# Optimization experiments

Measured on AMD Instinct MI355X. Metric: run time of the kernel, lower is better.

Reference implementation:

```python
import jax, jax.numpy as jnp
import numpy as np

N, E, IN_DIM, OUT_DIM, H = 50000, 800000, 128, 16, 8


def setup_inputs() -> dict:
    key = jax.random.key(0)
    ks = jax.random.split(key, 10)
    h = jax.random.normal(ks[0], (N, IN_DIM), dtype=jnp.float32)
    row = jnp.sort(jax.random.randint(ks[1], (E,), 0, N))
    col = jax.random.randint(ks[2], (E,), 0, N)
    s = 1.0 / np.sqrt(IN_DIM)
    Wq = jax.random.normal(ks[3], (IN_DIM, OUT_DIM * H), dtype=jnp.float32) * s
    Wk = jax.random.normal(ks[4], (IN_DIM, OUT_DIM * H), dtype=jnp.float32) * s
    Wv = jax.random.normal(ks[5], (IN_DIM, OUT_DIM * H), dtype=jnp.float32) * s
    bq = jnp.zeros((OUT_DIM * H,), jnp.float32)
    bk = jnp.zeros((OUT_DIM * H,), jnp.float32)
    bv = jnp.zeros((OUT_DIM * H,), jnp.float32)
    return {"h": h, "Wq": Wq, "bq": bq, "Wk": Wk, "bk": bk, "Wv": Wv, "bv": bv,
            "row": row, "col": col}


def reference(h, Wq, bq, Wk, bk, Wv, bv, row, col):
    n = h.shape[0]
    scaling = OUT_DIM ** (-0.5)
    # projections, reshaped (N, out_dim, heads) as in the torch module
    q = (h @ Wq + bq).reshape(n, OUT_DIM, H) * scaling
    k = (h @ Wk + bk).reshape(n, OUT_DIM, H)
    v = (h @ Wv + bv).reshape(n, OUT_DIM, H)
    # bsddmm: per-edge, per-head dot product  score[e,h] = <q[row[e],:,h], k[col[e],:,h]>
    s = jnp.einsum('edh,edh->eh', q[row], k[col])  # [E, H]
    # sparse row-wise softmax (over each destination node's neighbors)
    m = jax.ops.segment_max(s, row, num_segments=n)       # [N, H]
    p = jnp.exp(s - m[row])                               # [E, H]
    z = jax.ops.segment_sum(p, row, num_segments=n)       # [N, H]
    attn = p / z[row]                                     # [E, H]
    # bspmm: out[i,d,h] = sum_{e: row[e]=i} attn[e,h] * v[col[e],d,h]
    out = jax.ops.segment_sum(attn[:, None, :] * v[col], row, num_segments=n)
    return out.reshape(n, -1)
```

## Files before the change

### kernel.cpp

```cpp
#include <hip/hip_runtime.h>
#include <math.h>

typedef unsigned int uint32;
typedef _Float16 f16x8 __attribute__((ext_vector_type(8)));
typedef _Float16 f16x2 __attribute__((ext_vector_type(2)));
typedef float f32x4 __attribute__((ext_vector_type(4)));

union frag_u { f16x8 h; uint32 u[4]; uint4 q; };


__device__ __forceinline__ uint32 pack_f16(float lo, float hi) {
    auto r = __builtin_amdgcn_cvt_pkrtz(lo, hi);
    return __builtin_bit_cast(uint32, r);
}
__device__ __forceinline__ float dot2acc(uint32 a, uint32 b, float c) {
#if __has_builtin(__builtin_amdgcn_fdot2)
    return __builtin_amdgcn_fdot2(__builtin_bit_cast(f16x2, a),
                                  __builtin_bit_cast(f16x2, b), c, false);
#else
    f16x2 av = __builtin_bit_cast(f16x2, a), bv = __builtin_bit_cast(f16x2, b);
    return fmaf((float)av[0], (float)bv[0], fmaf((float)av[1], (float)bv[1], c));
#endif
}

__global__ __launch_bounds__(256) void proj_mfma_kernel(
    const float* __restrict__ h,
    const float* __restrict__ Wq, const float* __restrict__ Wk,
    const float* __restrict__ Wv,
    const float* __restrict__ bq, const float* __restrict__ bk,
    const float* __restrict__ bv,
    uint32* __restrict__ Qp, uint2* __restrict__ KV,
    const int* __restrict__ row, int* __restrict__ rp,
    int N, int E, int PB)
{
    const int t = threadIdx.x;
    if ((int)blockIdx.x >= PB) {
        int i = ((int)blockIdx.x - PB) * 256 + t;
        if (i > N) return;
        int lo = 0, hi = E;
        while (lo < hi) {
            int mid = (lo + hi) >> 1;
            if (row[mid] < i) lo = mid + 1; else hi = mid;
        }
        rp[i] = lo;
        return;
    }

    __shared__ uint32 Wl[8192];

    const int lane = t & 63;
    const int w = t >> 6;
    const int r = lane & 15, g = lane >> 4;
    const int rbase = blockIdx.x * 128 + w * 32;

    frag_u afr[2][4];
    const float4* h4 = reinterpret_cast<const float4*>(h);
    #pragma unroll
    for (int ng = 0; ng < 2; ++ng) {
        int arow = rbase + ng * 16 + r;
        bool av = arow < N;
        #pragma unroll
        for (int kb = 0; kb < 4; ++kb) {
            float4 x = make_float4(0.f,0.f,0.f,0.f), y = x;
            if (av) {
                size_t base = (size_t)arow * 32 + (kb * 4 + g) * 2;
                x = h4[base]; y = h4[base + 1];
            }
            afr[ng][kb].u[0] = pack_f16(x.x, x.y);
            afr[ng][kb].u[1] = pack_f16(x.z, x.w);
            afr[ng][kb].u[2] = pack_f16(y.x, y.y);
            afr[ng][kb].u[3] = pack_f16(y.z, y.w);
        }
    }

    const float SCALE_Q = 0.25f * 1.44269504f;
    uint32 kpk[4][2][4];

    #pragma unroll
    for (int mat = 0; mat < 3; ++mat) {
        const float* W = (mat == 0) ? Wq : (mat == 1) ? Wk : Wv;
        const float* bias = (mat == 0) ? bq : (mat == 1) ? bk : bv;

        __syncthreads();
        {
            const float4* W4 = reinterpret_cast<const float4*>(W);
            #pragma unroll
            for (int i0 = 0; i0 < 8; ++i0) {
                int i = t + i0 * 256;
                int k2 = i >> 5, nq = i & 31;
                float4 a = W4[(k2 * 2) * 32 + nq];
                float4 b = W4[(k2 * 2 + 1) * 32 + nq];
                int slot = k2 >> 2, rem = k2 & 3;
                #pragma unroll
                for (int e = 0; e < 4; ++e) {
                    int n = nq * 4 + e;
                    float lo = (e == 0) ? a.x : (e == 1) ? a.y : (e == 2) ? a.z : a.w;
                    float hi = (e == 0) ? b.x : (e == 1) ? b.y : (e == 2) ? b.z : b.w;
                    Wl[n * 64 + ((slot ^ (n & 7)) << 2) + rem] = pack_f16(lo, hi);
                }
            }
        }
        __syncthreads();

        #pragma unroll
        for (int tp = 0; tp < 4; ++tp) {
            const int c = tp * 16 + r;

            frag_u bfr[2][4];
            #pragma unroll
            for (int tti = 0; tti < 2; ++tti)
                #pragma unroll
                for (int kb = 0; kb < 4; ++kb) {
                    int n = (tp + 4 * tti) * 16 + r;
                    int s = kb * 4 + g;
                    bfr[tti][kb].q = *reinterpret_cast<const uint4*>(
                        &Wl[n * 64 + ((s ^ (n & 7)) << 2)]);
                }

            f32x4 acc[2][2];
            #pragma unroll
            for (int ng = 0; ng < 2; ++ng)
                #pragma unroll
                for (int tti = 0; tti < 2; ++tti)
                    acc[ng][tti] = (f32x4){0.f, 0.f, 0.f, 0.f};

            #pragma unroll
            for (int ng = 0; ng < 2; ++ng)
                #pragma unroll
                for (int tti = 0; tti < 2; ++tti)
                    #pragma unroll
                    for (int kb = 0; kb < 4; ++kb)
                        acc[ng][tti] = __builtin_amdgcn_mfma_f32_16x16x32_f16(
                            afr[ng][kb].h, bfr[tti][kb].h, acc[ng][tti], 0, 0, 0);

            float blo = bias[c], bhi = bias[c + 64];
            #pragma unroll
            for (int ng = 0; ng < 2; ++ng) {
                #pragma unroll
                for (int reg = 0; reg < 4; ++reg) {
                    int node = rbase + ng * 16 + g * 4 + reg;
                    float lo = acc[ng][0][reg] + blo;
                    float hi = acc[ng][1][reg] + bhi;
                    if (mat == 0) {
                        if (node < N)
                            Qp[(size_t)node * 64 + c] = pack_f16(lo * SCALE_Q, hi * SCALE_Q);
                    } else if (mat == 1) {
                        kpk[tp][ng][reg] = pack_f16(lo, hi);
                    } else {
                        if (node < N)
                            KV[(size_t)node * 64 + c] =
                                make_uint2(kpk[tp][ng][reg], pack_f16(lo, hi));
                    }
                }
            }
        }
    }
}

__global__ __launch_bounds__(128) void edge_attn_kernel(
    const uint32* __restrict__ Qp, const uint2* __restrict__ KV,
    const int* __restrict__ rp, const int* __restrict__ col,
    float* __restrict__ out, int N)
{
    const int lane = threadIdx.x & 63;
    const int node = blockIdx.x * 2 + (threadIdx.x >> 6);
    if (node >= N) return;
    const int hh   = lane & 7;
    const int slot = lane >> 3;

    const int start = rp[node], end = rp[node + 1];
    float* outp = out + (size_t)node * 128;
    if (start >= end) { outp[lane] = 0.f; outp[lane + 64] = 0.f; return; }
    const int last = end - 1;

    uint32 q[8];
    {
        const uint32* qrow = Qp + (size_t)node * 64;
        #pragma unroll
        for (int i = 0; i < 8; ++i) q[i] = qrow[hh + 8 * i];
    }

    float z = 0.f;
    float acc[16];
    #pragma unroll
    for (int i = 0; i < 16; ++i) acc[i] = 0.f;

    uint2 bufA[8], bufB[8];
    #define LOADG(buf, c0) { \
        const uint2* kvr = KV + (size_t)(c0) * 64; \
        _Pragma("unroll") \
        for (int i = 0; i < 8; ++i) (buf)[i] = kvr[hh + 8 * i]; }
    #define PROC(buf, gb) { \
        float s = 0.f; \
        _Pragma("unroll") \
        for (int i = 0; i < 8; ++i) s = dot2acc(q[i], (buf)[i].x, s); \
        float p = ((gb) + slot < end) ? __builtin_amdgcn_exp2f(s) : 0.f; \
        z += p; \
        _Pragma("unroll") \
        for (int i = 0; i < 8; ++i) { \
            f16x2 hv = __builtin_bit_cast(f16x2, (buf)[i].y); \
            acc[i]     = fmaf(p, (float)hv[0], acc[i]); \
            acc[8 + i] = fmaf(p, (float)hv[1], acc[8 + i]); } }

    int cA = col[min(start + slot, last)];
    int cB = col[min(start + 8 + slot, last)];
    LOADG(bufA, cA);
    int gb = start;
    while (true) {
        LOADG(bufB, cB);
        cA = col[min(gb + 16 + slot, last)];
        PROC(bufA, gb);
        gb += 8;
        if (gb >= end) break;
        LOADG(bufA, cA);
        cB = col[min(gb + 16 + slot, last)];
        PROC(bufB, gb);
        gb += 8;
        if (gb >= end) break;
    }

    #pragma unroll
    for (int m = 8; m <= 32; m <<= 1) {
        z += __shfl_xor(z, m);
        #pragma unroll
        for (int i = 0; i < 16; ++i) acc[i] += __shfl_xor(acc[i], m);
    }

    const float rz = 1.0f / z;
    outp[lane]      = acc[slot] * rz;
    outp[lane + 64] = acc[8 + slot] * rz;
}

extern "C" void kernel_launch(void* const* d_in, const int* in_sizes, int n_in,
                              void* d_out, int out_size, void* d_ws, size_t ws_size,
                              hipStream_t stream)
{
    const float* h  = (const float*)d_in[0];
    const float* Wq = (const float*)d_in[1];
    const float* bq = (const float*)d_in[2];
    const float* Wk = (const float*)d_in[3];
    const float* bk = (const float*)d_in[4];
    const float* Wv = (const float*)d_in[5];
    const float* bv = (const float*)d_in[6];
    const int* row  = (const int*)d_in[7];
    const int* col  = (const int*)d_in[8];
    float* out = (float*)d_out;

    const int N = in_sizes[0] / 128;
    const int E = in_sizes[7];

    uint2*  KV = (uint2*)d_ws;
    uint32* Qp = (uint32*)(KV + (size_t)N * 64);
    int*    rp = (int*)(Qp + (size_t)N * 64);

    const int PB = (N + 127) / 128;
    const int rp_blocks = (N + 1 + 255) / 256;

    proj_mfma_kernel<<<PB + rp_blocks, 256, 0, stream>>>(
        h, Wq, Wk, Wv, bq, bk, bv, Qp, KV, row, rp, N, E, PB);
    edge_attn_kernel<<<(N + 1) / 2, 128, 0, stream>>>(Qp, KV, rp, col, out, N);
}
```

Measured before the change: 89.92 us.

## Permute Q/KV layout for 128-bit loads and process two nodes per wavefront

Measured after the change: 96.71 us. 7.5% more time.

```diff
diff --git a/kernel.cpp b/kernel.cpp
--- a/kernel.cpp
+++ b/kernel.cpp
@@ -105,6 +105,7 @@
         #pragma unroll
         for (int tp = 0; tp < 4; ++tp) {
             const int c = tp * 16 + r;
+            const int pc = ((c & 7) << 3) | (c >> 3);
 
             frag_u bfr[2][4];
             #pragma unroll
@@ -143,12 +144,12 @@
                     float hi = acc[ng][1][reg] + bhi;
                     if (mat == 0) {
                         if (node < N)
-                            Qp[(size_t)node * 64 + c] = pack_f16(lo * SCALE_Q, hi * SCALE_Q);
+                            Qp[(size_t)node * 64 + pc] = pack_f16(lo * SCALE_Q, hi * SCALE_Q);
                     } else if (mat == 1) {
                         kpk[tp][ng][reg] = pack_f16(lo, hi);
                     } else {
                         if (node < N)
-                            KV[(size_t)node * 64 + c] =
+                            KV[(size_t)node * 64 + pc] =
                                 make_uint2(kpk[tp][ng][reg], pack_f16(lo, hi));
                     }
                 }
@@ -158,26 +159,40 @@
 }
 
 __global__ __launch_bounds__(128) void edge_attn_kernel(
-    const uint32* __restrict__ Qp, const uint2* __restrict__ KV,
+    const uint4* __restrict__ Qp4, const uint4* __restrict__ KV4,
     const int* __restrict__ rp, const int* __restrict__ col,
     float* __restrict__ out, int N)
 {
     const int lane = threadIdx.x & 63;
-    const int node = blockIdx.x * 2 + (threadIdx.x >> 6);
-    if (node >= N) return;
+    const int wid  = blockIdx.x * 2 + (threadIdx.x >> 6);
+    const int half = lane >> 5;
+    const int node = wid * 2 + half;
     const int hh   = lane & 7;
-    const int slot = lane >> 3;
-
-    const int start = rp[node], end = rp[node + 1];
-    float* outp = out + (size_t)node * 128;
-    if (start >= end) { outp[lane] = 0.f; outp[lane + 64] = 0.f; return; }
-    const int last = end - 1;
+    const int slot = (lane >> 3) & 3;
+    const bool valid = node < N;
+
+    const int start = valid ? rp[node] : 0;
+    const int end   = valid ? rp[node + 1] : 0;
+    const int deg = end - start;
+
+    int cnt = (deg + 3) >> 2;
+    { int o = __shfl_xor(cnt, 32); cnt = cnt > o ? cnt : o; }
+    if (cnt == 0) {
+        if (valid) {
+            float* outp = out + (size_t)node * 128;
+            int b = lane & 31;
+            outp[b] = 0.f; outp[b + 32] = 0.f; outp[b + 64] = 0.f; outp[b + 96] = 0.f;
+        }
+        return;
+    }
+    const int lastc = (deg > 0) ? end - 1 : 0;
 
     uint32 q[8];
     {
-        const uint32* qrow = Qp + (size_t)node * 64;
-        #pragma unroll
-        for (int i = 0; i < 8; ++i) q[i] = qrow[hh + 8 * i];
+        const uint4* qrow = Qp4 + ((size_t)(valid ? node : 0) * 16 + hh * 2);
+        uint4 qa = qrow[0], qb = qrow[1];
+        q[0]=qa.x; q[1]=qa.y; q[2]=qa.z; q[3]=qa.w;
+        q[4]=qb.x; q[5]=qb.y; q[6]=qb.z; q[7]=qb.w;
     }
 
     float z = 0.f;
@@ -185,50 +200,59 @@
     #pragma unroll
     for (int i = 0; i < 16; ++i) acc[i] = 0.f;
 
-    uint2 bufA[8], bufB[8];
+    uint4 bufA[4], bufB[4];
     #define LOADG(buf, c0) { \
-        const uint2* kvr = KV + (size_t)(c0) * 64; \
-        _Pragma("unroll") \
-        for (int i = 0; i < 8; ++i) (buf)[i] = kvr[hh + 8 * i]; }
-    #define PROC(buf, gb) { \
+        const uint4* kvr = KV4 + ((size_t)(c0) * 32 + hh * 4); \
+        buf[0] = kvr[0]; buf[1] = kvr[1]; buf[2] = kvr[2]; buf[3] = kvr[3]; }
+    #define PROC(buf, e) { \
         float s = 0.f; \
-        _Pragma("unroll") \
-        for (int i = 0; i < 8; ++i) s = dot2acc(q[i], (buf)[i].x, s); \
-        float p = ((gb) + slot < end) ? __builtin_amdgcn_exp2f(s) : 0.f; \
+        s = dot2acc(q[0], buf[0].x, s); s = dot2acc(q[1], buf[0].z, s); \
+        s = dot2acc(q[2], buf[1].x, s); s = dot2acc(q[3], buf[1].z, s); \
+        s = dot2acc(q[4], buf[2].x, s); s = dot2acc(q[5], buf[2].z, s); \
+        s = dot2acc(q[6], buf[3].x, s); s = dot2acc(q[7], buf[3].z, s); \
+        float p = ((e) < end) ? __builtin_amdgcn_exp2f(s) : 0.f; \
         z += p; \
         _Pragma("unroll") \
-        for (int i = 0; i < 8; ++i) { \
-            f16x2 hv = __builtin_bit_cast(f16x2, (buf)[i].y); \
-            acc[i]     = fmaf(p, (float)hv[0], acc[i]); \
-            acc[8 + i] = fmaf(p, (float)hv[1], acc[8 + i]); } }
-
-    int cA = col[min(start + slot, last)];
-    int cB = col[min(start + 8 + slot, last)];
+        for (int j = 0; j < 4; ++j) { \
+            f16x2 v0 = __builtin_bit_cast(f16x2, buf[j].y); \
+            f16x2 v1 = __builtin_bit_cast(f16x2, buf[j].w); \
+            acc[2*j]     = fmaf(p, (float)v0[0], acc[2*j]); \
+            acc[2*j+8]   = fmaf(p, (float)v0[1], acc[2*j+8]); \
+            acc[2*j+1]   = fmaf(p, (float)v1[0], acc[2*j+1]); \
+            acc[2*j+9]   = fmaf(p, (float)v1[1], acc[2*j+9]); } }
+
+    const int e0 = start + slot;
+    int cA = col[min(e0, lastc)];
     LOADG(bufA, cA);
-    int gb = start;
+    int cB = col[min(e0 + 4, lastc)];
+    int it = 0;
     while (true) {
         LOADG(bufB, cB);
-        cA = col[min(gb + 16 + slot, last)];
-        PROC(bufA, gb);
-        gb += 8;
-        if (gb >= end) break;
+        cA = col[min(e0 + (it + 2) * 4, lastc)];
+        PROC(bufA, e0 + it * 4);
+        ++it; if (it >= cnt) break;
         LOADG(bufA, cA);
-        cB = col[min(gb + 16 + slot, last)];
-        PROC(bufB, gb);
-        gb += 8;
-        if (gb >= end) break;
-    }
-
-    #pragma unroll
-    for (int m = 8; m <= 32; m <<= 1) {
+        cB = col[min(e0 + (it + 2) * 4, lastc)];
+        PROC(bufB, e0 + it * 4);
+        ++it; if (it >= cnt) break;
+    }
+
+    #pragma unroll
+    for (int m = 8; m <= 16; m <<= 1) {
         z += __shfl_xor(z, m);
         #pragma unroll
         for (int i = 0; i < 16; ++i) acc[i] += __shfl_xor(acc[i], m);
     }
 
-    const float rz = 1.0f / z;
-    outp[lane]      = acc[slot] * rz;
-    outp[lane + 64] = acc[8 + slot] * rz;
+    const float rz = (z > 0.f) ? 1.0f / z : 0.f;
+    if (valid) {
+        float* outp = out + (size_t)node * 128;
+        int b = lane & 31;
+        outp[b]      = acc[slot]      * rz;
+        outp[b + 32] = acc[slot + 4]  * rz;
+        outp[b + 64] = acc[slot + 8]  * rz;
+        outp[b + 96] = acc[slot + 12] * rz;
+    }
 }
 
 extern "C" void kernel_launch(void* const* d_in, const int* in_sizes, int n_in,
@@ -258,5 +282,6 @@
 
     proj_mfma_kernel<<<PB + rp_blocks, 256, 0, stream>>>(
         h, Wq, Wk, Wv, bq, bk, bv, Qp, KV, row, rp, N, E, PB);
-    edge_attn_kernel<<<(N + 1) / 2, 128, 0, stream>>>(Qp, KV, rp, col, out, N);
-}
+    edge_attn_kernel<<<(N + 3) / 4, 128, 0, stream>>>(
+        (const uint4*)Qp, (const uint4*)KV, rp, col, out, N);
+}
```
